# Kernel tuning notes

Measured on AMD Instinct MI355X. Metric: run time of the kernel, lower is better.

The kernel has to match this reference:

```python
import jax, jax.numpy as jnp
import numpy as np

N_NODES = 50000
N_EDGES = 640000
DIMS = [128, 256, 128]


def setup_inputs() -> dict:
    key = jax.random.key(0)
    ks = jax.random.split(key, 8)
    x = jax.random.normal(ks[0], (N_NODES, DIMS[0]), dtype=jnp.float32)
    src = jax.random.randint(ks[1], (N_EDGES,), 0, N_NODES)
    dst = jax.random.randint(ks[2], (N_EDGES,), 0, N_NODES)
    # ensure no pre-existing self loops so add_remaining_self_loops == append all loops
    dst = jnp.where(dst == src, (dst + 1) % N_NODES, dst)
    edge_index = jnp.stack([src, dst]).astype(jnp.int64)
    # SAGEConv lin_l weights (root_weight=False -> only neighbor linear), Kaiming-ish init
    def lin(k, fan_in, fan_out):
        s = 1.0 / np.sqrt(fan_in)
        kw, kb = jax.random.split(k)
        W = jax.random.uniform(kw, (fan_out, fan_in), minval=-s, maxval=s, dtype=jnp.float32)
        b = jax.random.uniform(kb, (fan_out,), minval=-s, maxval=s, dtype=jnp.float32)
        return W, b
    W1, b1 = lin(ks[3], DIMS[0], DIMS[1])
    W2, b2 = lin(ks[4], DIMS[1], DIMS[2])
    logit_scale = jnp.asarray(np.log(1.0 / 0.07), dtype=jnp.float32)
    return {"x": x, "edge_index": edge_index, "W1": W1, "b1": b1,
            "W2": W2, "b2": b2, "logit_scale": logit_scale}


def reference(x, edge_index, W1, b1, W2, b2, logit_scale):
    N = x.shape[0]
    loops = jnp.arange(N, dtype=edge_index.dtype)
    src = jnp.concatenate([edge_index[0], loops])  # add_remaining_self_loops
    dst = jnp.concatenate([edge_index[1], loops])
    deg = jax.ops.segment_sum(jnp.ones_like(dst, dtype=x.dtype), dst, num_segments=N)
    inv_deg = 1.0 / deg  # deg >= 1 thanks to self loops

    def sage_conv(y, W, b):
        # mean aggregation of source features at destination, then linear
        agg = jax.ops.segment_sum(y[src], dst, num_segments=N) * inv_deg[:, None]
        return agg @ W.T + b

    y = jax.nn.relu(sage_conv(x, W1, b1))
    y = sage_conv(y, W2, b2)
    # F.normalize(p=2, dim=-1, eps=1e-12)
    nrm = jnp.maximum(jnp.linalg.norm(y, axis=-1, keepdims=True), 1e-12)
    y = y / nrm
    return y * jnp.exp(logit_scale)
```

## Files before the change

### kernel.cpp

```cpp
#include <hip/hip_runtime.h>
#include <hip/hip_bf16.h>

#define N_NODES 50000
#define NPAD 50048
#define ZROW N_NODES
#define D0 128
#define D1 256
#define D2 128
#define N4 1600000
#define NB4 1601536
#define CAP 64
#define PPB 52

typedef __attribute__((ext_vector_type(8))) short short8;
typedef __attribute__((ext_vector_type(8))) unsigned short ushort8;
typedef __attribute__((ext_vector_type(4))) float f32x4;

static __device__ __forceinline__ unsigned short f2bf(float f) {
    __hip_bfloat16 h = __float2bfloat16(f);
    return *(unsigned short*)&h;
}
static __device__ __forceinline__ float bf2f(unsigned short u) {
    return __uint_as_float(((unsigned int)u) << 16);
}

__global__ __launch_bounds__(256) void k_prep(const float* __restrict__ x,
                                              unsigned short* __restrict__ x_bf,
                                              const float* __restrict__ W1,
                                              const float* __restrict__ W2,
                                              unsigned short* __restrict__ W1p,
                                              unsigned short* __restrict__ W2p,
                                              const int* __restrict__ ei,
                                              int* __restrict__ cursor,
                                              unsigned short* __restrict__ csr, int E) {
    __shared__ int s_is64;
    if (threadIdx.x < 64) {
        int lane = threadIdx.x;
        int nz = 0;
#pragma unroll
        for (int k = 0; k < 4; k++) nz += (ei[2 * (lane * 4 + k) + 1] != 0);
#pragma unroll
        for (int off = 32; off > 0; off >>= 1) nz += __shfl_down(nz, off, 64);
        if (lane == 0) s_is64 = (nz == 0) ? 1 : 0;
    }
    __syncthreads();
    int idx = blockIdx.x * 256 + threadIdx.x;

    if (threadIdx.x < PPB) {
        int p = blockIdx.x * PPB + threadIdx.x;
        if (2 * p < E) {
            int is64 = s_is64;
            int es0, ed0, es1, ed1;
            if (is64) {
                int4 sp = ((const int4*)ei)[p];
                int4 dp = ((const int4*)(ei + 2 * (size_t)E))[p];
                es0 = sp.x; es1 = sp.z; ed0 = dp.x; ed1 = dp.z;
            } else {
                int2 sp = ((const int2*)ei)[p];
                int2 dp = ((const int2*)(ei + (size_t)E))[p];
                es0 = sp.x; es1 = sp.y; ed0 = dp.x; ed1 = dp.y;
            }
            int p0 = atomicAdd(&cursor[ed0], 1);
            if (p0 < CAP) csr[(size_t)ed0 * CAP + p0] = (unsigned short)es0;
            if (2 * p + 1 < E) {
                int p1 = atomicAdd(&cursor[ed1], 1);
                if (p1 < CAP) csr[(size_t)ed1 * CAP + p1] = (unsigned short)es1;
            }
        }
    }

    if (idx < N4) {
        float4 v = ((const float4*)x)[idx];
        ushort4 u;
        u.x = f2bf(v.x); u.y = f2bf(v.y); u.z = f2bf(v.z); u.w = f2bf(v.w);
        ((ushort4*)x_bf)[idx] = u;
    } else if (idx < NB4) {
        ushort4 z = {0, 0, 0, 0};
        ((ushort4*)x_bf)[idx] = z;
    }

    if (idx < 2 * D0 * D1) {
        if (idx < D0 * D1) {
            int j = idx & 7, lane = (idx >> 3) & 63, tile = idx >> 9;
            int ct = tile & 15, kt = tile >> 4;
            int k = kt * 32 + (lane >> 4) * 8 + j;
            int n = ct * 16 + (lane & 15);
            W1p[idx] = f2bf(W1[n * D0 + k]);
        } else {
            int i2 = idx - D0 * D1;
            int j = i2 & 7, lane = (i2 >> 3) & 63, tile = i2 >> 9;
            int ct = tile & 7, kt = tile >> 3;
            int k = kt * 32 + (lane >> 4) * 8 + j;
            int n = ct * 16 + (lane & 15);
            W2p[i2] = f2bf(W2[n * D1 + k]);
        }
    }
}

#define A_LD 132
#define H_LD 260
__global__ __launch_bounds__(256, 6) void k_gmlp(const unsigned short* __restrict__ x_bf,
                                                 const unsigned short* __restrict__ csr,
                                                 const int* __restrict__ cursor,
                                                 const unsigned short* __restrict__ W1p,
                                                 const float* __restrict__ b1,
                                                 const unsigned short* __restrict__ W2p,
                                                 unsigned short* __restrict__ t_bf) {
    __shared__ unsigned short Abuf[16 * A_LD];
    __shared__ unsigned short Hbuf[16 * H_LD];
    int tid = threadIdx.x;
    int n0 = blockIdx.x * 16;

    {
        int g = tid >> 4, h = tid & 15;
        int node = n0 + g;
        unsigned short* lp = Abuf + g * A_LD + h * 8;
        if (node < N_NODES) {
            int dg = cursor[node]; if (dg > CAP) dg = CAP;
            const unsigned short* cp = csr + (size_t)node * CAP;
            ushort8 u = *(const ushort8*)(x_bf + (size_t)node * 128 + h * 8);
            ushort8 c0 = ((const ushort8*)cp)[0];
            ushort8 c1 = ((const ushort8*)cp)[1];
            int idx[16];
#pragma unroll
            for (int u8 = 0; u8 < 8; u8++) { idx[u8] = c0[u8]; idx[8 + u8] = c1[u8]; }
#pragma unroll
            for (int u8 = 0; u8 < 16; u8++)
                if (u8 >= dg) idx[u8] = ZROW;
            ushort8 rr[16];
#pragma unroll
            for (int u8 = 0; u8 < 16; u8++)
                rr[u8] = *(const ushort8*)(x_bf + (size_t)idx[u8] * 128 + h * 8);
            float a0[8], a1[8];
#pragma unroll
            for (int t = 0; t < 8; t++) { a0[t] = bf2f(u[t]); a1[t] = 0.f; }
#pragma unroll
            for (int t = 0; t < 8; t++) {
                a0[t] += bf2f(rr[0][t]) + bf2f(rr[2][t]) + bf2f(rr[4][t]) + bf2f(rr[6][t])
                       + bf2f(rr[8][t]) + bf2f(rr[10][t]) + bf2f(rr[12][t]) + bf2f(rr[14][t]);
                a1[t] += bf2f(rr[1][t]) + bf2f(rr[3][t]) + bf2f(rr[5][t]) + bf2f(rr[7][t])
                       + bf2f(rr[9][t]) + bf2f(rr[11][t]) + bf2f(rr[13][t]) + bf2f(rr[15][t]);
            }
            for (int j = 16; j < dg; j += 8) {
                int idx2[8];
#pragma unroll
                for (int u8 = 0; u8 < 8; u8++) {
                    int jj = j + u8;
                    idx2[u8] = (jj < dg) ? (int)cp[jj] : ZROW;
                }
                ushort8 r2[8];
#pragma unroll
                for (int u8 = 0; u8 < 8; u8++)
                    r2[u8] = *(const ushort8*)(x_bf + (size_t)idx2[u8] * 128 + h * 8);
#pragma unroll
                for (int t = 0; t < 8; t++) {
                    a0[t] += bf2f(r2[0][t]) + bf2f(r2[2][t]) + bf2f(r2[4][t]) + bf2f(r2[6][t]);
                    a1[t] += bf2f(r2[1][t]) + bf2f(r2[3][t]) + bf2f(r2[5][t]) + bf2f(r2[7][t]);
                }
            }
            float invd = 1.0f / (float)(dg + 1);
            ushort8 o;
#pragma unroll
            for (int t = 0; t < 8; t++) o[t] = f2bf((a0[t] + a1[t]) * invd);
            *(ushort8*)lp = o;
        } else {
            ushort8 z = {0, 0, 0, 0, 0, 0, 0, 0};
            *(ushort8*)lp = z;
        }
    }
    __syncthreads();

    int w = tid >> 6, lane = tid & 63;
    int m = lane & 15, q = lane >> 4;

    {
        short8 af[4];
        const unsigned short* arow = Abuf + m * A_LD + q * 8;
#pragma unroll
        for (int kt = 0; kt < 4; kt++) af[kt] = *(const short8*)(arow + kt * 32);
#pragma unroll
        for (int c = 0; c < 4; c++) {
            int ct = w * 4 + c;
            f32x4 acc = {0.f, 0.f, 0.f, 0.f};
#pragma unroll
            for (int kt = 0; kt < 4; kt++) {
                short8 bw = *(const short8*)(W1p + (((kt * 16 + ct) * 64 + lane) << 3));
                acc = __builtin_amdgcn_mfma_f32_16x16x32_bf16(af[kt], bw, acc, 0, 0, 0);
            }
            int col = ct * 16 + m;
            float bias = b1[col];
#pragma unroll
            for (int r = 0; r < 4; r++)
                Hbuf[(q * 4 + r) * H_LD + col] = f2bf(fmaxf(acc[r] + bias, 0.0f));
        }
    }
    __syncthreads();

    {
        short8 hf[8];
        const unsigned short* hrow = Hbuf + m * H_LD + q * 8;
#pragma unroll
        for (int kt = 0; kt < 8; kt++) hf[kt] = *(const short8*)(hrow + kt * 32);
#pragma unroll
        for (int c = 0; c < 2; c++) {
            int ct = w * 2 + c;
            f32x4 acc = {0.f, 0.f, 0.f, 0.f};
#pragma unroll
            for (int kt = 0; kt < 8; kt++) {
                short8 bw = *(const short8*)(W2p + (((kt * 8 + ct) * 64 + lane) << 3));
                acc = __builtin_amdgcn_mfma_f32_16x16x32_bf16(hf[kt], bw, acc, 0, 0, 0);
            }
            int col = ct * 16 + m;
#pragma unroll
            for (int r = 0; r < 4; r++) {
                int node = n0 + q * 4 + r;
                t_bf[(size_t)node * 128 + col] = (node < N_NODES) ? f2bf(acc[r]) : (unsigned short)0;
            }
        }
    }
}

__global__ __launch_bounds__(256) void k_gather_final(const unsigned short* __restrict__ t,
                                                      const unsigned short* __restrict__ csr,
                                                      const int* __restrict__ cursor,
                                                      const float* __restrict__ b2,
                                                      const float* __restrict__ ls,
                                                      float* __restrict__ out) {
    int tid = threadIdx.x;
    int h = tid & 15;
    int node = blockIdx.x * 16 + (tid >> 4);

    int dg = cursor[node]; if (dg > CAP) dg = CAP;
    const unsigned short* cp = csr + (size_t)node * CAP;
    ushort8 u = *(const ushort8*)(t + (size_t)node * 128 + h * 8);
    ushort8 c0 = ((const ushort8*)cp)[0];
    ushort8 c1 = ((const ushort8*)cp)[1];
    int idx[16];
#pragma unroll
    for (int u8 = 0; u8 < 8; u8++) { idx[u8] = c0[u8]; idx[8 + u8] = c1[u8]; }
#pragma unroll
    for (int u8 = 0; u8 < 16; u8++)
        if (u8 >= dg) idx[u8] = ZROW;
    ushort8 rr[16];
#pragma unroll
    for (int u8 = 0; u8 < 16; u8++)
        rr[u8] = *(const ushort8*)(t + (size_t)idx[u8] * 128 + h * 8);
    float a0[8], a1[8];
#pragma unroll
    for (int k = 0; k < 8; k++) { a0[k] = bf2f(u[k]); a1[k] = 0.f; }
#pragma unroll
    for (int k = 0; k < 8; k++) {
        a0[k] += bf2f(rr[0][k]) + bf2f(rr[2][k]) + bf2f(rr[4][k]) + bf2f(rr[6][k])
               + bf2f(rr[8][k]) + bf2f(rr[10][k]) + bf2f(rr[12][k]) + bf2f(rr[14][k]);
        a1[k] += bf2f(rr[1][k]) + bf2f(rr[3][k]) + bf2f(rr[5][k]) + bf2f(rr[7][k])
               + bf2f(rr[9][k]) + bf2f(rr[11][k]) + bf2f(rr[13][k]) + bf2f(rr[15][k]);
    }
    for (int j = 16; j < dg; j += 8) {
        int idx2[8];
#pragma unroll
        for (int u8 = 0; u8 < 8; u8++) {
            int jj = j + u8;
            idx2[u8] = (jj < dg) ? (int)cp[jj] : ZROW;
        }
        ushort8 r2[8];
#pragma unroll
        for (int u8 = 0; u8 < 8; u8++)
            r2[u8] = *(const ushort8*)(t + (size_t)idx2[u8] * 128 + h * 8);
#pragma unroll
        for (int k = 0; k < 8; k++) {
            a0[k] += bf2f(r2[0][k]) + bf2f(r2[2][k]) + bf2f(r2[4][k]) + bf2f(r2[6][k]);
            a1[k] += bf2f(r2[1][k]) + bf2f(r2[3][k]) + bf2f(r2[5][k]) + bf2f(r2[7][k]);
        }
    }
    float invd = 1.0f / (float)(dg + 1);
    float4 bb0 = ((const float4*)b2)[h * 2];
    float4 bb1 = ((const float4*)b2)[h * 2 + 1];
    float v[8];
    v[0] = (a0[0] + a1[0]) * invd + bb0.x;
    v[1] = (a0[1] + a1[1]) * invd + bb0.y;
    v[2] = (a0[2] + a1[2]) * invd + bb0.z;
    v[3] = (a0[3] + a1[3]) * invd + bb0.w;
    v[4] = (a0[4] + a1[4]) * invd + bb1.x;
    v[5] = (a0[5] + a1[5]) * invd + bb1.y;
    v[6] = (a0[6] + a1[6]) * invd + bb1.z;
    v[7] = (a0[7] + a1[7]) * invd + bb1.w;

    float s = 0.f;
#pragma unroll
    for (int k = 0; k < 8; k++) s += v[k] * v[k];
#pragma unroll
    for (int msk = 8; msk > 0; msk >>= 1) s += __shfl_xor(s, msk, 64);
    float nrm = fmaxf(sqrtf(s), 1e-12f);
    float scale = expf(ls[0]) / nrm;
    float4 o0, o1;
    o0.x = v[0] * scale; o0.y = v[1] * scale; o0.z = v[2] * scale; o0.w = v[3] * scale;
    o1.x = v[4] * scale; o1.y = v[5] * scale; o1.z = v[6] * scale; o1.w = v[7] * scale;
    float* op = out + (size_t)node * 128 + h * 8;
    *(float4*)(op + 0) = o0;
    *(float4*)(op + 4) = o1;
}

extern "C" void kernel_launch(void* const* d_in, const int* in_sizes, int n_in,
                              void* d_out, int out_size, void* d_ws, size_t ws_size,
                              hipStream_t stream) {
    const float* x  = (const float*)d_in[0];
    const int*   ei = (const int*)d_in[1];
    const float* W1 = (const float*)d_in[2];
    const float* b1 = (const float*)d_in[3];
    const float* W2 = (const float*)d_in[4];
    const float* b2 = (const float*)d_in[5];
    const float* ls = (const float*)d_in[6];
    float* out = (float*)d_out;

    const int E = in_sizes[1] / 2;

    char* ws = (char*)d_ws;
    size_t off = 0;
    auto alloc = [&](size_t bytes) {
        size_t o = off;
        off = (off + bytes + 255) & ~(size_t)255;
        return o;
    };
    int*            cursor = (int*)(ws + alloc((size_t)N_NODES * 4));
    unsigned short* csr    = (unsigned short*)(ws + alloc((size_t)N_NODES * CAP * 2));
    unsigned short* W1p    = (unsigned short*)(ws + alloc((size_t)D0 * D1 * 2));
    unsigned short* W2p    = (unsigned short*)(ws + alloc((size_t)D1 * D2 * 2));
    unsigned short* x_bf   = (unsigned short*)(ws + alloc((size_t)NPAD * D0 * 2));
    unsigned short* t_bf   = (unsigned short*)(ws + alloc((size_t)NPAD * D2 * 2));

    hipMemsetAsync(cursor, 0, (size_t)N_NODES * 4, stream);
    k_prep<<<(NB4 + 255) / 256, 256, 0, stream>>>(x, x_bf, W1, W2, W1p, W2p, ei, cursor, csr, E);
    k_gmlp<<<NPAD / 16, 256, 0, stream>>>(x_bf, csr, cursor, W1p, b1, W2p, t_bf);
    k_gather_final<<<N_NODES / 16, 256, 0, stream>>>(t_bf, csr, cursor, b2, ls, out);
}
```

Baseline: 188.8 us.

## Process 32 nodes per block and reuse weight fragments across two row tiles

The fused gather+MLP kernel now runs 512 threads on 32 nodes per block instead of 256 threads on 16. In both GEMMs each wave loads its weight fragments once and applies them to two 16-row tiles, reading the activation fragments from LDS per tile. This halves the global/L2 weight traffic per node. The cost is doubled LDS per block and higher register pressure under the tighter launch bound, which may reduce occupancy.

```diff
diff --git a/kernel.cpp b/kernel.cpp
--- a/kernel.cpp
+++ b/kernel.cpp
@@ -99,17 +99,17 @@
 
 #define A_LD 132
 #define H_LD 260
-__global__ __launch_bounds__(256, 6) void k_gmlp(const unsigned short* __restrict__ x_bf,
+__global__ __launch_bounds__(512, 8) void k_gmlp(const unsigned short* __restrict__ x_bf,
                                                  const unsigned short* __restrict__ csr,
                                                  const int* __restrict__ cursor,
                                                  const unsigned short* __restrict__ W1p,
                                                  const float* __restrict__ b1,
                                                  const unsigned short* __restrict__ W2p,
                                                  unsigned short* __restrict__ t_bf) {
-    __shared__ unsigned short Abuf[16 * A_LD];
-    __shared__ unsigned short Hbuf[16 * H_LD];
+    __shared__ unsigned short Abuf[32 * A_LD];
+    __shared__ unsigned short Hbuf[32 * H_LD];
     int tid = threadIdx.x;
-    int n0 = blockIdx.x * 16;
+    int n0 = blockIdx.x * 32;
 
     {
         int g = tid >> 4, h = tid & 15;
@@ -174,46 +174,50 @@
     int m = lane & 15, q = lane >> 4;
 
     {
-        short8 af[4];
-        const unsigned short* arow = Abuf + m * A_LD + q * 8;
-#pragma unroll
-        for (int kt = 0; kt < 4; kt++) af[kt] = *(const short8*)(arow + kt * 32);
-#pragma unroll
-        for (int c = 0; c < 4; c++) {
-            int ct = w * 4 + c;
-            f32x4 acc = {0.f, 0.f, 0.f, 0.f};
-#pragma unroll
-            for (int kt = 0; kt < 4; kt++) {
-                short8 bw = *(const short8*)(W1p + (((kt * 16 + ct) * 64 + lane) << 3));
-                acc = __builtin_amdgcn_mfma_f32_16x16x32_bf16(af[kt], bw, acc, 0, 0, 0);
-            }
+#pragma unroll
+        for (int c2 = 0; c2 < 2; c2++) {
+            int ct = w + c2 * 8;
+            short8 bw[4];
+#pragma unroll
+            for (int kt = 0; kt < 4; kt++)
+                bw[kt] = *(const short8*)(W1p + (((kt * 16 + ct) * 64 + lane) << 3));
             int col = ct * 16 + m;
             float bias = b1[col];
 #pragma unroll
-            for (int r = 0; r < 4; r++)
-                Hbuf[(q * 4 + r) * H_LD + col] = f2bf(fmaxf(acc[r] + bias, 0.0f));
+            for (int rt = 0; rt < 2; rt++) {
+                const unsigned short* arow = Abuf + (rt * 16 + m) * A_LD + q * 8;
+                f32x4 acc = {0.f, 0.f, 0.f, 0.f};
+#pragma unroll
+                for (int kt = 0; kt < 4; kt++) {
+                    short8 af = *(const short8*)(arow + kt * 32);
+                    acc = __builtin_amdgcn_mfma_f32_16x16x32_bf16(af, bw[kt], acc, 0, 0, 0);
+                }
+#pragma unroll
+                for (int r = 0; r < 4; r++)
+                    Hbuf[(rt * 16 + q * 4 + r) * H_LD + col] = f2bf(fmaxf(acc[r] + bias, 0.0f));
+            }
         }
     }
     __syncthreads();
 
     {
-        short8 hf[8];
-        const unsigned short* hrow = Hbuf + m * H_LD + q * 8;
-#pragma unroll
-        for (int kt = 0; kt < 8; kt++) hf[kt] = *(const short8*)(hrow + kt * 32);
-#pragma unroll
-        for (int c = 0; c < 2; c++) {
-            int ct = w * 2 + c;
+        short8 bw2[8];
+#pragma unroll
+        for (int kt = 0; kt < 8; kt++)
+            bw2[kt] = *(const short8*)(W2p + (((kt * 8 + w) * 64 + lane) << 3));
+        int col = w * 16 + m;
+#pragma unroll
+        for (int rt = 0; rt < 2; rt++) {
+            const unsigned short* hrow = Hbuf + (rt * 16 + m) * H_LD + q * 8;
             f32x4 acc = {0.f, 0.f, 0.f, 0.f};
 #pragma unroll
             for (int kt = 0; kt < 8; kt++) {
-                short8 bw = *(const short8*)(W2p + (((kt * 8 + ct) * 64 + lane) << 3));
-                acc = __builtin_amdgcn_mfma_f32_16x16x32_bf16(hf[kt], bw, acc, 0, 0, 0);
-            }
-            int col = ct * 16 + m;
+                short8 hf = *(const short8*)(hrow + kt * 32);
+                acc = __builtin_amdgcn_mfma_f32_16x16x32_bf16(hf, bw2[kt], acc, 0, 0, 0);
+            }
 #pragma unroll
             for (int r = 0; r < 4; r++) {
-                int node = n0 + q * 4 + r;
+                int node = n0 + rt * 16 + q * 4 + r;
                 t_bf[(size_t)node * 128 + col] = (node < N_NODES) ? f2bf(acc[r]) : (unsigned short)0;
             }
         }
@@ -330,6 +334,6 @@
 
     hipMemsetAsync(cursor, 0, (size_t)N_NODES * 4, stream);
     k_prep<<<(NB4 + 255) / 256, 256, 0, stream>>>(x, x_bf, W1, W2, W1p, W2p, ei, cursor, csr, E);
-    k_gmlp<<<NPAD / 16, 256, 0, stream>>>(x_bf, csr, cursor, W1p, b1, W2p, t_bf);
+    k_gmlp<<<NPAD / 32, 512, 0, stream>>>(x_bf, csr, cursor, W1p, b1, W2p, t_bf);
     k_gather_final<<<N_NODES / 16, 256, 0, stream>>>(t_bf, csr, cursor, b2, ls, out);
 }
```

Measured after the change: 237.3 us. +25.7%, slower.
